# Performance work log

Hardware: AMD Instinct MI355X
Metric: run time of the kernel (lower is better)

Reference implementation:

```python
import jax, jax.numpy as jnp
import numpy as np

N_PP = 100000   # papers
N_A = 50000     # authors
N_AP = N_PP + N_A
DIM = 16
B = 8192        # sampled node set sizes
E = 500000      # edges per modality
ALPHA = 0.5
EPS = 1e-12


def _cdist(x, y):
    # Euclidean cdist via quadratic expansion (avoids [N,M,d] intermediate)
    sq = (jnp.sum(x * x, -1)[:, None] + jnp.sum(y * y, -1)[None, :]
          - 2.0 * x @ y.T)
    return jnp.sqrt(jnp.maximum(sq, EPS))


def _pdist(x, y):
    d = x - y
    return jnp.sqrt(jnp.sum(d * d, -1) + EPS)


def setup_inputs() -> dict:
    key = jax.random.key(0)
    ks = jax.random.split(key, 10)
    u = lambda k, s: jax.random.uniform(k, s, jnp.float32, -1.0, 1.0)  # 2*rand-1
    p = u(ks[0], (N_PP, DIM))
    p_star = u(ks[1], (N_PP, DIM))
    a = u(ks[2], (N_A, DIM))
    beta_ap = u(ks[3], (N_AP,))
    gamma_pp = u(ks[4], (2 * N_PP,))
    edges_pp = jax.random.randint(ks[5], (2, E), 0, N_PP, jnp.int32)
    e_ap0 = jax.random.randint(ks[6], (1, E), 0, N_PP, jnp.int32)
    e_ap1 = jax.random.randint(ks[7], (1, E), N_PP, N_AP, jnp.int32)
    edges_ap = jnp.concatenate([e_ap0, e_ap1], 0)
    p_star_nodes = jnp.sort(jax.random.randint(ks[8], (B,), 0, N_PP, jnp.int32))
    kk = jax.random.split(ks[9], 2)
    p_nodes = jax.random.randint(kk[0], (B,), 0, N_PP, jnp.int32)
    a_nodes = jax.random.randint(kk[1], (B,), N_PP, N_AP, jnp.int32)
    return {"p": p, "p_star": p_star, "a": a, "beta_ap": beta_ap,
            "gamma_pp": gamma_pp, "edges_pp": edges_pp, "edges_ap": edges_ap,
            "p_star_nodes": p_star_nodes, "p_nodes": p_nodes, "a_nodes": a_nodes}


def reference(p, p_star, a, beta_ap, gamma_pp,
              edges_pp, edges_ap, p_star_nodes, p_nodes, a_nodes):
    # ---- pp modality ----
    # link term over edges (edges[0]=p_star idx, edges[1]=p idx)
    link_pp = jnp.sum(gamma_pp[edges_pp[0]] + gamma_pp[edges_pp[1] + N_PP]
                      - _pdist(p_star[edges_pp[0]], p[edges_pp[1]]))
    # non-link term: [B_pstar, B_p] matrix, upper-triangular (k=1) masked sum
    g_ps = gamma_pp[p_star_nodes]                 # [B]
    g_p = gamma_pp[p_nodes + N_PP]                # [B]
    mat_pp = g_ps[:, None] + g_p[None, :]         # == gamma_mat.T in torch code
    dist_pp = _cdist(p_star[p_star_nodes], p[p_nodes])
    nonlink_pp = jnp.sum(jnp.triu(jnp.exp(mat_pp - dist_pp), k=1))
    nll_pp = -(link_pp - nonlink_pp)

    # ---- ap modality ----
    link_ap = jnp.sum(beta_ap[edges_ap[0]] + beta_ap[edges_ap[1]]
                      - _pdist(p_star[edges_ap[0]], a[edges_ap[1] - N_PP]))
    b_ps = beta_ap[p_star_nodes]
    b_a = beta_ap[a_nodes]
    mat_ap = b_ps[:, None] + b_a[None, :]         # == beta_mat.T
    dist_ap = _cdist(p_star[p_star_nodes], a[a_nodes - N_PP])
    nonlink_ap = jnp.sum(jnp.exp(mat_ap - dist_ap))
    nll_ap = -(link_ap - nonlink_ap)

    # average batch loss as in __train_one_batch
    loss = ALPHA * nll_pp / B + (1.0 - ALPHA) * nll_ap / B
    return loss
```

## Files before the change

### kernel.cpp

```cpp
#include <hip/hip_runtime.h>

#define N_PP 100000
#define N_A  50000
#define NEDGE 500000
#define BSZ 8192
#define TILE 128
#define SCALE 1.44269504088896f

#define GRID_F 1024
#define PAIR_JOBS 8192
#define EDGE_JOBS 489
#define NJOBS (PAIR_JOBS + EDGE_JOBS)

typedef __attribute__((ext_vector_type(8)))  short bf16x8;
typedef __attribute__((ext_vector_type(16))) float f32x16;
typedef __attribute__((ext_vector_type(4)))  float f32x4;
typedef unsigned short u16;

#if __has_builtin(__builtin_amdgcn_sqrtf)
#define FAST_SQRT(x) __builtin_amdgcn_sqrtf(x)
#else
#define FAST_SQRT(x) sqrtf(x)
#endif
#if __has_builtin(__builtin_amdgcn_exp2f)
#define FAST_EXP2(x) __builtin_amdgcn_exp2f(x)
#else
#define FAST_EXP2(x) exp2f(x)
#endif

__device__ __forceinline__ u16 f2bf(float f) {
    unsigned u = __builtin_bit_cast(unsigned, f);
    u += 0x7FFFu + ((u >> 16) & 1u);
    return (u16)(u >> 16);
}
__device__ __forceinline__ float bf2f(u16 s) {
    unsigned u = ((unsigned)s) << 16;
    return __builtin_bit_cast(float, u);
}

__device__ __forceinline__ bf16x8 load_frag_f32(const float* __restrict__ src) {
    float4 v0 = *(const float4*)src;
    float4 v1 = *(const float4*)(src + 4);
    bf16x8 f;
    f[0] = (short)f2bf(v0.x); f[1] = (short)f2bf(v0.y);
    f[2] = (short)f2bf(v0.z); f[3] = (short)f2bf(v0.w);
    f[4] = (short)f2bf(v1.x); f[5] = (short)f2bf(v1.y);
    f[6] = (short)f2bf(v1.z); f[7] = (short)f2bf(v1.w);
    return f;
}

__device__ __forceinline__ float pdist16_bf(const u16* __restrict__ xr,
                                            const u16* __restrict__ yr) {
    bf16x8 x0 = *(const bf16x8*)xr, x1 = *(const bf16x8*)(xr + 8);
    bf16x8 y0 = *(const bf16x8*)yr, y1 = *(const bf16x8*)(yr + 8);
    float d2 = 1e-12f;
#pragma unroll
    for (int i = 0; i < 8; ++i) {
        float dx = bf2f((u16)x0[i]) - bf2f((u16)y0[i]); d2 = fmaf(dx, dx, d2);
        float dy = bf2f((u16)x1[i]) - bf2f((u16)y1[i]); d2 = fmaf(dy, dy, d2);
    }
    return sqrtf(d2);
}

__device__ __forceinline__ float pdist16_f32(const float* __restrict__ xv,
                                             const float* __restrict__ yv) {
    float d2 = 1e-12f;
#pragma unroll
    for (int c = 0; c < 16; c += 4) {
        float4 xq = *(const float4*)(xv + c);
        float4 yq = *(const float4*)(yv + c);
        float dx = xq.x - yq.x; d2 = fmaf(dx, dx, d2);
        float dy = xq.y - yq.y; d2 = fmaf(dy, dy, d2);
        float dz = xq.z - yq.z; d2 = fmaf(dz, dz, d2);
        float dw = xq.w - yq.w; d2 = fmaf(dw, dw, d2);
    }
    return sqrtf(d2);
}

__global__ __launch_bounds__(256) void prep_kernel(
        const float* __restrict__ p, const float* __restrict__ p_star,
        const float* __restrict__ a, const float* __restrict__ beta,
        const float* __restrict__ gamma,
        const int* __restrict__ psn, const int* __restrict__ pn,
        const int* __restrict__ an,
        u16* __restrict__ ps_tab, u16* __restrict__ p_tab, u16* __restrict__ a_tab,
        u16* __restrict__ Xb, u16* __restrict__ Yp, u16* __restrict__ Ya,
        float* __restrict__ Xxx, float* __restrict__ Xg,
        float* __restrict__ Pyy, float* __restrict__ Pg,
        float* __restrict__ Ayy, float* __restrict__ Ag)
{
    const int NITEMS = 250000 + 3 * BSZ;
    for (int i = blockIdx.x * 256 + threadIdx.x; i < NITEMS; i += gridDim.x * 256) {
        if (i < 250000) {
            const float* src; u16* dst;
            if (i < 100000)      { src = p_star + (size_t)i * 16;       dst = ps_tab + (size_t)i * 16; }
            else if (i < 200000) { src = p + (size_t)(i - 100000) * 16; dst = p_tab + (size_t)(i - 100000) * 16; }
            else                 { src = a + (size_t)(i - 200000) * 16; dst = a_tab + (size_t)(i - 200000) * 16; }
            bf16x8 lo = load_frag_f32(src);
            bf16x8 hi = load_frag_f32(src + 8);
            *(bf16x8*)dst = lo;
            *(bf16x8*)(dst + 8) = hi;
        } else {
            const int j = i - 250000;
            const int which = j >> 13;
            const int r = j & (BSZ - 1);
            const float* src; float wsc; u16* drow; float* xxp; float* gp;
            if (which == 0) {
                int node = psn[r]; src = p_star + (size_t)node * 16;
                wsc = gamma[node] * SCALE; drow = Xb + (size_t)r * 16; xxp = Xxx; gp = Xg;
            } else if (which == 1) {
                int node = pn[r]; src = p + (size_t)node * 16;
                wsc = gamma[node + N_PP] * SCALE; drow = Yp + (size_t)r * 16; xxp = Pyy; gp = Pg;
            } else {
                int node = an[r]; src = a + (size_t)(node - N_PP) * 16;
                wsc = beta[node] * SCALE; drow = Ya + (size_t)r * 16; xxp = Ayy; gp = Ag;
            }
            bf16x8 lo = load_frag_f32(src);
            bf16x8 hi = load_frag_f32(src + 8);
            *(bf16x8*)drow = lo;
            *(bf16x8*)(drow + 8) = hi;
            float ss = 0.f;
#pragma unroll
            for (int c = 0; c < 8; ++c) {
                float q0 = bf2f((u16)lo[c]); ss = fmaf(q0, q0, ss);
                float q1 = bf2f((u16)hi[c]); ss = fmaf(q1, q1, ss);
            }
            xxp[r] = ss;
            gp[r] = wsc;
        }
    }
}

template <bool DIAG>
__device__ __forceinline__ float epi_rt(
        const f32x16& ca, const f32x16& cb,
        const float* __restrict__ xxg, const float* __restrict__ gxg,
        int rb, float yy0, float gy0, float yy1, float gy1,
        int cj0, int cj1)
{
    f32x4 xxq[4], gxq[4];
#pragma unroll
    for (int q = 0; q < 4; ++q) {
        xxq[q] = *(const f32x4*)&xxg[rb + q * 8];
        gxq[q] = *(const f32x4*)&gxg[rb + q * 8];
    }
    float s = 0.f;
#pragma unroll
    for (int q = 0; q < 4; ++q) {
#pragma unroll
        for (int j = 0; j < 4; ++j) {
            const int reg = q * 4 + j;
            float sxy = xxq[q][j];
            float gx  = gxq[q][j];
            float sq0 = fmaf(-2.f, ca[reg], sxy + yy0);
            float d0  = FAST_SQRT(fmaxf(sq0, 1e-12f));
            float v0  = FAST_EXP2(fmaf(-SCALE, d0, gx + gy0));
            float sq1 = fmaf(-2.f, cb[reg], sxy + yy1);
            float d1  = FAST_SQRT(fmaxf(sq1, 1e-12f));
            float v1  = FAST_EXP2(fmaf(-SCALE, d1, gx + gy1));
            if (DIAG) {
                int row = rb + q * 8 + j;
                v0 = (cj0 > row) ? v0 : 0.f;
                v1 = (cj1 > row) ? v1 : 0.f;
            }
            s += v0 + v1;
        }
    }
    return s;
}

template <bool PACKED>
__global__ __launch_bounds__(256) void fused_kernel(
        const float* __restrict__ p, const float* __restrict__ p_star,
        const float* __restrict__ a, const float* __restrict__ beta,
        const float* __restrict__ gamma,
        const int* __restrict__ edges_pp, const int* __restrict__ edges_ap,
        const int* __restrict__ psn, const int* __restrict__ pn,
        const int* __restrict__ an,
        const u16* __restrict__ ps_tab, const u16* __restrict__ p_tab,
        const u16* __restrict__ a_tab,
        const u16* __restrict__ Xb, const u16* __restrict__ Yp,
        const u16* __restrict__ Ya,
        const float* __restrict__ Xxx, const float* __restrict__ Xg,
        const float* __restrict__ Pyy, const float* __restrict__ Pg,
        const float* __restrict__ Ayy, const float* __restrict__ Ag,
        float* __restrict__ partials)
{
    const int t = threadIdx.x;
    const int l = t & 63, w = t >> 6;
    const int wr = w >> 1, wc = w & 1;
    const int l31 = l & 31, h = l >> 5;

    __shared__ float sxx[TILE], sgx[TILE], syy[TILE], sgy[TILE];
    __shared__ float red4[4][4];

    float s_ppl = 0.f, s_ppn = 0.f, s_apl = 0.f, s_apn = 0.f;

    for (int j = blockIdx.x; j < NJOBS; j += gridDim.x) {
        if (j < PAIR_JOBS) {
            const bool pp = (j < 4096);
            const int jj = pp ? j : j - 4096;
            const int bx = jj & 63, by = jj >> 6;
            if (pp && bx < by) continue;
            const bool diag = pp && (bx == by);

            bf16x8 aF0, aF1, bF0, bF1;
            const float* xxg; const float* gxg;
            float yy0, gy0, yy1, gy1;
            const int cj0 = wc * 64 + l31, cj1 = cj0 + 32;
            const int rb0 = wr * 64 + 4 * h, rb1 = rb0 + 32;

            if (PACKED) {
                const u16* Ytab = pp ? Yp : Ya;
                const float* yyP = (pp ? Pyy : Ayy) + bx * TILE;
                const float* gyP = (pp ? Pg  : Ag ) + bx * TILE;
                const int ar0 = by * TILE + wr * 64 + l31;
                const int bc0 = bx * TILE + wc * 64 + l31;
                aF0 = *(const bf16x8*)(Xb   + (size_t)ar0 * 16 + h * 8);
                aF1 = *(const bf16x8*)(Xb   + (size_t)(ar0 + 32) * 16 + h * 8);
                bF0 = *(const bf16x8*)(Ytab + (size_t)bc0 * 16 + h * 8);
                bF1 = *(const bf16x8*)(Ytab + (size_t)(bc0 + 32) * 16 + h * 8);
                xxg = Xxx + by * TILE;
                gxg = Xg  + by * TILE;
                yy0 = yyP[cj0]; gy0 = gyP[cj0];
                yy1 = yyP[cj1]; gy1 = gyP[cj1];
            } else {
                const float* Y  = pp ? p : a;
                const float* wv = pp ? gamma : beta;
                const int* yn   = pp ? pn : an;
                const int wyo   = pp ? N_PP : 0;
                const int yvo   = pp ? 0 : -N_PP;
                const int ar0 = by * TILE + wr * 64 + l31;
                const int an0 = psn[ar0], an1 = psn[ar0 + 32];
                aF0 = load_frag_f32(p_star + (size_t)an0 * 16 + h * 8);
                aF1 = load_frag_f32(p_star + (size_t)an1 * 16 + h * 8);
                const int bc0g = bx * TILE + wc * 64 + l31;
                const int bn0 = yn[bc0g], bn1 = yn[bc0g + 32];
                bF0 = load_frag_f32(Y + (size_t)(bn0 + yvo) * 16 + h * 8);
                bF1 = load_frag_f32(Y + (size_t)(bn1 + yvo) * 16 + h * 8);
                {
                    const bool isx = (t < 128);
                    const int  r   = isx ? t : t - 128;
                    const int  node = isx ? psn[by * TILE + r] : yn[bx * TILE + r];
                    const float* src = isx ? (p_star + (size_t)node * 16)
                                           : (Y + (size_t)(node + yvo) * 16);
                    float ss = 0.f;
#pragma unroll
                    for (int c = 0; c < 16; c += 4) {
                        float4 v = *(const float4*)(src + c);
                        float q0 = bf2f(f2bf(v.x)), q1 = bf2f(f2bf(v.y));
                        float q2 = bf2f(f2bf(v.z)), q3 = bf2f(f2bf(v.w));
                        ss = fmaf(q0, q0, ss); ss = fmaf(q1, q1, ss);
                        ss = fmaf(q2, q2, ss); ss = fmaf(q3, q3, ss);
                    }
                    if (isx) { sxx[r] = ss; sgx[r] = wv[node] * SCALE; }
                    else     { syy[r] = ss; sgy[r] = wv[node + wyo] * SCALE; }
                }
                __syncthreads();
                xxg = sxx; gxg = sgx;
                yy0 = syy[cj0]; gy0 = sgy[cj0];
                yy1 = syy[cj1]; gy1 = sgy[cj1];
            }

            f32x16 c00, c01, c10, c11;
#pragma unroll
            for (int i = 0; i < 16; ++i) { c00[i] = 0.f; c01[i] = 0.f; c10[i] = 0.f; c11[i] = 0.f; }
            c00 = __builtin_amdgcn_mfma_f32_32x32x16_bf16(aF0, bF0, c00, 0, 0, 0);
            c01 = __builtin_amdgcn_mfma_f32_32x32x16_bf16(aF0, bF1, c01, 0, 0, 0);
            c10 = __builtin_amdgcn_mfma_f32_32x32x16_bf16(aF1, bF0, c10, 0, 0, 0);
            c11 = __builtin_amdgcn_mfma_f32_32x32x16_bf16(aF1, bF1, c11, 0, 0, 0);

            float sum;
            if (diag) {
                sum = epi_rt<true >(c00, c01, xxg, gxg, rb0, yy0, gy0, yy1, gy1, cj0, cj1)
                    + epi_rt<true >(c10, c11, xxg, gxg, rb1, yy0, gy0, yy1, gy1, cj0, cj1);
            } else {
                sum = epi_rt<false>(c00, c01, xxg, gxg, rb0, yy0, gy0, yy1, gy1, cj0, cj1)
                    + epi_rt<false>(c10, c11, xxg, gxg, rb1, yy0, gy0, yy1, gy1, cj0, cj1);
            }
            if (pp) s_ppn += sum; else s_apn += sum;
            if (!PACKED) __syncthreads();
        } else {
            const int base = (j - PAIR_JOBS) * 1024;
#pragma unroll 2
            for (int k = 0; k < 4; ++k) {
                int i = base + k * 256 + t;
                if (i < NEDGE) {
                    int e0 = edges_pp[i], e1 = edges_pp[NEDGE + i];
                    int f0 = edges_ap[i], f1 = edges_ap[NEDGE + i];
                    if (PACKED) {
                        s_ppl += gamma[e0] + gamma[e1 + N_PP]
                               - pdist16_bf(ps_tab + (size_t)e0 * 16, p_tab + (size_t)e1 * 16);
                        s_apl += beta[f0] + beta[f1]
                               - pdist16_bf(ps_tab + (size_t)f0 * 16, a_tab + (size_t)(f1 - N_PP) * 16);
                    } else {
                        s_ppl += gamma[e0] + gamma[e1 + N_PP]
                               - pdist16_f32(p_star + (size_t)e0 * 16, p + (size_t)e1 * 16);
                        s_apl += beta[f0] + beta[f1]
                               - pdist16_f32(p_star + (size_t)f0 * 16, a + (size_t)(f1 - N_PP) * 16);
                    }
                }
            }
        }
    }

    float v4[4] = {s_ppl, s_ppn, s_apl, s_apn};
#pragma unroll
    for (int c = 0; c < 4; ++c) {
        float r = v4[c];
#pragma unroll
        for (int o = 32; o > 0; o >>= 1) r += __shfl_down(r, o, 64);
        if (l == 0) red4[w][c] = r;
    }
    __syncthreads();
    if (t < 4)
        partials[(size_t)blockIdx.x * 4 + t] =
            red4[0][t] + red4[1][t] + red4[2][t] + red4[3][t];
}

__global__ __launch_bounds__(256) void finalize_kernel(
        const float* __restrict__ partials, float* __restrict__ out)
{
    __shared__ double acc4[4];
    const int t = threadIdx.x;
    const int c = t >> 6, l = t & 63;
    double s = 0.0;
    for (int i = l; i < GRID_F; i += 64) s += (double)partials[(size_t)i * 4 + c];
#pragma unroll
    for (int o = 32; o > 0; o >>= 1) s += __shfl_down(s, o, 64);
    if (l == 0) acc4[c] = s;
    __syncthreads();
    if (t == 0) {
        double nll_pp = -(acc4[0] - acc4[1]);
        double nll_ap = -(acc4[2] - acc4[3]);
        out[0] = (float)(0.5 * nll_pp / (double)BSZ + 0.5 * nll_ap / (double)BSZ);
    }
}

extern "C" void kernel_launch(void* const* d_in, const int* in_sizes, int n_in,
                              void* d_out, int out_size, void* d_ws, size_t ws_size,
                              hipStream_t stream)
{
    const float* p       = (const float*)d_in[0];
    const float* p_star  = (const float*)d_in[1];
    const float* a       = (const float*)d_in[2];
    const float* beta    = (const float*)d_in[3];
    const float* gamma   = (const float*)d_in[4];
    const int* edges_pp  = (const int*)d_in[5];
    const int* edges_ap  = (const int*)d_in[6];
    const int* psn       = (const int*)d_in[7];
    const int* pn        = (const int*)d_in[8];
    const int* an        = (const int*)d_in[9];

    char* ws = (char*)d_ws;
    size_t off = 0;
    float* partials = (float*)(ws + off); off += (size_t)GRID_F * 4 * sizeof(float);
    u16* ps_tab = (u16*)(ws + off); off += (size_t)100000 * 32;
    u16* p_tab  = (u16*)(ws + off); off += (size_t)100000 * 32;
    u16* a_tab  = (u16*)(ws + off); off += (size_t)50000 * 32;
    u16* Xb     = (u16*)(ws + off); off += (size_t)BSZ * 32;
    u16* Yp     = (u16*)(ws + off); off += (size_t)BSZ * 32;
    u16* Ya     = (u16*)(ws + off); off += (size_t)BSZ * 32;
    float* Xxx  = (float*)(ws + off); off += BSZ * 4;
    float* Xg   = (float*)(ws + off); off += BSZ * 4;
    float* Pyy  = (float*)(ws + off); off += BSZ * 4;
    float* Pg   = (float*)(ws + off); off += BSZ * 4;
    float* Ayy  = (float*)(ws + off); off += BSZ * 4;
    float* Ag   = (float*)(ws + off); off += BSZ * 4;
    const bool packed = (ws_size >= off);

    if (packed) {
        prep_kernel<<<256, 256, 0, stream>>>(
            p, p_star, a, beta, gamma, psn, pn, an,
            ps_tab, p_tab, a_tab, Xb, Yp, Ya, Xxx, Xg, Pyy, Pg, Ayy, Ag);
        fused_kernel<true><<<GRID_F, 256, 0, stream>>>(
            p, p_star, a, beta, gamma, edges_pp, edges_ap, psn, pn, an,
            ps_tab, p_tab, a_tab, Xb, Yp, Ya, Xxx, Xg, Pyy, Pg, Ayy, Ag, partials);
    } else {
        fused_kernel<false><<<GRID_F, 256, 0, stream>>>(
            p, p_star, a, beta, gamma, edges_pp, edges_ap, psn, pn, an,
            nullptr, nullptr, nullptr, nullptr, nullptr, nullptr,
            nullptr, nullptr, nullptr, nullptr, nullptr, nullptr, partials);
    }

    finalize_kernel<<<1, 256, 0, stream>>>(partials, (float*)d_out);
}
```

Baseline: 85.83 us.

## Quantize gathered edge embeddings to int8 with sdot4 and rebalance job schedule

The edge-link term now gathers rows quantized to int8 (16 bytes per row instead of 32) and computes distances with sdot4 integer dot products, roughly halving gather traffic for the one million random edge lookups. The job list is reordered so edge jobs come first with smaller 512-edge chunks. The pp upper-triangle tiles are enumerated directly through a triangular index mapping instead of being skipped. Grid size doubles and launch bounds request 4 blocks per SM. Int8 quantization with scale 127 adds distance error of roughly 1e-2 per element, which may exceed the tolerance. Distances also lose the epsilon floor, so sqrt(0) is possible.

```diff
diff --git a/kernel.cpp b/kernel.cpp
--- a/kernel.cpp
+++ b/kernel.cpp
@@ -6,11 +6,14 @@
 #define BSZ 8192
 #define TILE 128
 #define SCALE 1.44269504088896f
-
-#define GRID_F 1024
-#define PAIR_JOBS 8192
-#define EDGE_JOBS 489
-#define NJOBS (PAIR_JOBS + EDGE_JOBS)
+#define QS 127.0f
+#define QSI (1.0f / 127.0f)
+
+#define GRID_F 2048
+#define EDGE_JOBS 977
+#define PP_JOBS 2080
+#define AP_JOBS 4096
+#define NJOBS (EDGE_JOBS + PP_JOBS + AP_JOBS)
 
 typedef __attribute__((ext_vector_type(8)))  short bf16x8;
 typedef __attribute__((ext_vector_type(16))) float f32x16;
@@ -49,17 +52,39 @@
     return f;
 }
 
-__device__ __forceinline__ float pdist16_bf(const u16* __restrict__ xr,
-                                            const u16* __restrict__ yr) {
-    bf16x8 x0 = *(const bf16x8*)xr, x1 = *(const bf16x8*)(xr + 8);
-    bf16x8 y0 = *(const bf16x8*)yr, y1 = *(const bf16x8*)(yr + 8);
-    float d2 = 1e-12f;
-#pragma unroll
-    for (int i = 0; i < 8; ++i) {
-        float dx = bf2f((u16)x0[i]) - bf2f((u16)y0[i]); d2 = fmaf(dx, dx, d2);
-        float dy = bf2f((u16)x1[i]) - bf2f((u16)y1[i]); d2 = fmaf(dy, dy, d2);
-    }
-    return sqrtf(d2);
+__device__ __forceinline__ int dot4i8(int a, int b, int c) {
+#if __has_builtin(__builtin_amdgcn_sdot4)
+    return __builtin_amdgcn_sdot4(a, b, c, false);
+#else
+    int s = c;
+#pragma unroll
+    for (int k = 0; k < 4; ++k) {
+        int av = (int)(signed char)(a >> (8 * k));
+        int bv = (int)(signed char)(b >> (8 * k));
+        s += av * bv;
+    }
+    return s;
+#endif
+}
+
+__device__ __forceinline__ float dist_i8(const int* __restrict__ ra,
+                                         const int* __restrict__ rb) {
+    int4 qa = *(const int4*)ra;
+    int4 qb = *(const int4*)rb;
+    int dot = dot4i8(qa.x, qb.x, 0);
+    dot = dot4i8(qa.y, qb.y, dot);
+    dot = dot4i8(qa.z, qb.z, dot);
+    dot = dot4i8(qa.w, qb.w, dot);
+    int na = dot4i8(qa.x, qa.x, 0);
+    na = dot4i8(qa.y, qa.y, na);
+    na = dot4i8(qa.z, qa.z, na);
+    na = dot4i8(qa.w, qa.w, na);
+    int nb = dot4i8(qb.x, qb.x, 0);
+    nb = dot4i8(qb.y, qb.y, nb);
+    nb = dot4i8(qb.z, qb.z, nb);
+    nb = dot4i8(qb.w, qb.w, nb);
+    int d2 = na + nb - 2 * dot;
+    return FAST_SQRT((float)d2) * QSI;
 }
 
 __device__ __forceinline__ float pdist16_f32(const float* __restrict__ xv,
@@ -77,13 +102,20 @@
     return sqrtf(d2);
 }
 
+__device__ __forceinline__ unsigned packq4(float a, float b, float c, float d) {
+    int qa = (int)rintf(a * QS), qb = (int)rintf(b * QS);
+    int qc = (int)rintf(c * QS), qd = (int)rintf(d * QS);
+    return (unsigned)(qa & 0xFF) | ((unsigned)(qb & 0xFF) << 8)
+         | ((unsigned)(qc & 0xFF) << 16) | ((unsigned)(qd & 0xFF) << 24);
+}
+
 __global__ __launch_bounds__(256) void prep_kernel(
         const float* __restrict__ p, const float* __restrict__ p_star,
         const float* __restrict__ a, const float* __restrict__ beta,
         const float* __restrict__ gamma,
         const int* __restrict__ psn, const int* __restrict__ pn,
         const int* __restrict__ an,
-        u16* __restrict__ ps_tab, u16* __restrict__ p_tab, u16* __restrict__ a_tab,
+        int* __restrict__ ps8, int* __restrict__ p8, int* __restrict__ a8,
         u16* __restrict__ Xb, u16* __restrict__ Yp, u16* __restrict__ Ya,
         float* __restrict__ Xxx, float* __restrict__ Xg,
         float* __restrict__ Pyy, float* __restrict__ Pg,
@@ -92,14 +124,20 @@
     const int NITEMS = 250000 + 3 * BSZ;
     for (int i = blockIdx.x * 256 + threadIdx.x; i < NITEMS; i += gridDim.x * 256) {
         if (i < 250000) {
-            const float* src; u16* dst;
-            if (i < 100000)      { src = p_star + (size_t)i * 16;       dst = ps_tab + (size_t)i * 16; }
-            else if (i < 200000) { src = p + (size_t)(i - 100000) * 16; dst = p_tab + (size_t)(i - 100000) * 16; }
-            else                 { src = a + (size_t)(i - 200000) * 16; dst = a_tab + (size_t)(i - 200000) * 16; }
-            bf16x8 lo = load_frag_f32(src);
-            bf16x8 hi = load_frag_f32(src + 8);
-            *(bf16x8*)dst = lo;
-            *(bf16x8*)(dst + 8) = hi;
+            const float* src; int* dst;
+            if (i < 100000)      { src = p_star + (size_t)i * 16;       dst = ps8 + (size_t)i * 4; }
+            else if (i < 200000) { src = p + (size_t)(i - 100000) * 16; dst = p8 + (size_t)(i - 100000) * 4; }
+            else                 { src = a + (size_t)(i - 200000) * 16; dst = a8 + (size_t)(i - 200000) * 4; }
+            float4 v0 = *(const float4*)src;
+            float4 v1 = *(const float4*)(src + 4);
+            float4 v2 = *(const float4*)(src + 8);
+            float4 v3 = *(const float4*)(src + 12);
+            int4 q;
+            q.x = (int)packq4(v0.x, v0.y, v0.z, v0.w);
+            q.y = (int)packq4(v1.x, v1.y, v1.z, v1.w);
+            q.z = (int)packq4(v2.x, v2.y, v2.z, v2.w);
+            q.w = (int)packq4(v3.x, v3.y, v3.z, v3.w);
+            *(int4*)dst = q;
         } else {
             const int j = i - 250000;
             const int which = j >> 13;
@@ -170,15 +208,15 @@
 }
 
 template <bool PACKED>
-__global__ __launch_bounds__(256) void fused_kernel(
+__global__ __launch_bounds__(256, 4) void fused_kernel(
         const float* __restrict__ p, const float* __restrict__ p_star,
         const float* __restrict__ a, const float* __restrict__ beta,
         const float* __restrict__ gamma,
         const int* __restrict__ edges_pp, const int* __restrict__ edges_ap,
         const int* __restrict__ psn, const int* __restrict__ pn,
         const int* __restrict__ an,
-        const u16* __restrict__ ps_tab, const u16* __restrict__ p_tab,
-        const u16* __restrict__ a_tab,
+        const int* __restrict__ ps8, const int* __restrict__ p8,
+        const int* __restrict__ a8,
         const u16* __restrict__ Xb, const u16* __restrict__ Yp,
         const u16* __restrict__ Ya,
         const float* __restrict__ Xxx, const float* __restrict__ Xg,
@@ -197,11 +235,43 @@
     float s_ppl = 0.f, s_ppn = 0.f, s_apl = 0.f, s_apn = 0.f;
 
     for (int j = blockIdx.x; j < NJOBS; j += gridDim.x) {
-        if (j < PAIR_JOBS) {
-            const bool pp = (j < 4096);
-            const int jj = pp ? j : j - 4096;
-            const int bx = jj & 63, by = jj >> 6;
-            if (pp && bx < by) continue;
+        if (j < EDGE_JOBS) {
+            const int base = j * 512;
+#pragma unroll
+            for (int k = 0; k < 2; ++k) {
+                int i = base + k * 256 + t;
+                if (i < NEDGE) {
+                    int e0 = __builtin_nontemporal_load(edges_pp + i);
+                    int e1 = __builtin_nontemporal_load(edges_pp + NEDGE + i);
+                    int f0 = __builtin_nontemporal_load(edges_ap + i);
+                    int f1 = __builtin_nontemporal_load(edges_ap + NEDGE + i);
+                    if (PACKED) {
+                        s_ppl += gamma[e0] + gamma[e1 + N_PP]
+                               - dist_i8(ps8 + (size_t)e0 * 4, p8 + (size_t)e1 * 4);
+                        s_apl += beta[f0] + beta[f1]
+                               - dist_i8(ps8 + (size_t)f0 * 4, a8 + (size_t)(f1 - N_PP) * 4);
+                    } else {
+                        s_ppl += gamma[e0] + gamma[e1 + N_PP]
+                               - pdist16_f32(p_star + (size_t)e0 * 16, p + (size_t)e1 * 16);
+                        s_apl += beta[f0] + beta[f1]
+                               - pdist16_f32(p_star + (size_t)f0 * 16, a + (size_t)(f1 - N_PP) * 16);
+                    }
+                }
+            }
+        } else {
+            const bool pp = (j < EDGE_JOBS + PP_JOBS);
+            int bx, by;
+            if (pp) {
+                int k = j - EDGE_JOBS;
+                float disc = sqrtf((float)(129 * 129 - 8 * k));
+                by = (int)((129.0f - disc) * 0.5f);
+                while (64 * by - (by * (by - 1)) / 2 > k) --by;
+                while (64 * (by + 1) - ((by + 1) * by) / 2 <= k) ++by;
+                bx = by + (k - (64 * by - (by * (by - 1)) / 2));
+            } else {
+                int k = j - EDGE_JOBS - PP_JOBS;
+                bx = k & 63; by = k >> 6;
+            }
             const bool diag = pp && (bx == by);
 
             bf16x8 aF0, aF1, bF0, bF1;
@@ -280,27 +350,6 @@
             }
             if (pp) s_ppn += sum; else s_apn += sum;
             if (!PACKED) __syncthreads();
-        } else {
-            const int base = (j - PAIR_JOBS) * 1024;
-#pragma unroll 2
-            for (int k = 0; k < 4; ++k) {
-                int i = base + k * 256 + t;
-                if (i < NEDGE) {
-                    int e0 = edges_pp[i], e1 = edges_pp[NEDGE + i];
-                    int f0 = edges_ap[i], f1 = edges_ap[NEDGE + i];
-                    if (PACKED) {
-                        s_ppl += gamma[e0] + gamma[e1 + N_PP]
-                               - pdist16_bf(ps_tab + (size_t)e0 * 16, p_tab + (size_t)e1 * 16);
-                        s_apl += beta[f0] + beta[f1]
-                               - pdist16_bf(ps_tab + (size_t)f0 * 16, a_tab + (size_t)(f1 - N_PP) * 16);
-                    } else {
-                        s_ppl += gamma[e0] + gamma[e1 + N_PP]
-                               - pdist16_f32(p_star + (size_t)e0 * 16, p + (size_t)e1 * 16);
-                        s_apl += beta[f0] + beta[f1]
-                               - pdist16_f32(p_star + (size_t)f0 * 16, a + (size_t)(f1 - N_PP) * 16);
-                    }
-                }
-            }
         }
     }
 
@@ -355,27 +404,27 @@
     char* ws = (char*)d_ws;
     size_t off = 0;
     float* partials = (float*)(ws + off); off += (size_t)GRID_F * 4 * sizeof(float);
-    u16* ps_tab = (u16*)(ws + off); off += (size_t)100000 * 32;
-    u16* p_tab  = (u16*)(ws + off); off += (size_t)100000 * 32;
-    u16* a_tab  = (u16*)(ws + off); off += (size_t)50000 * 32;
-    u16* Xb     = (u16*)(ws + off); off += (size_t)BSZ * 32;
-    u16* Yp     = (u16*)(ws + off); off += (size_t)BSZ * 32;
-    u16* Ya     = (u16*)(ws + off); off += (size_t)BSZ * 32;
-    float* Xxx  = (float*)(ws + off); off += BSZ * 4;
-    float* Xg   = (float*)(ws + off); off += BSZ * 4;
-    float* Pyy  = (float*)(ws + off); off += BSZ * 4;
-    float* Pg   = (float*)(ws + off); off += BSZ * 4;
-    float* Ayy  = (float*)(ws + off); off += BSZ * 4;
-    float* Ag   = (float*)(ws + off); off += BSZ * 4;
+    int* ps8 = (int*)(ws + off); off += (size_t)100000 * 16;
+    int* p8  = (int*)(ws + off); off += (size_t)100000 * 16;
+    int* a8  = (int*)(ws + off); off += (size_t)50000 * 16;
+    u16* Xb  = (u16*)(ws + off); off += (size_t)BSZ * 32;
+    u16* Yp  = (u16*)(ws + off); off += (size_t)BSZ * 32;
+    u16* Ya  = (u16*)(ws + off); off += (size_t)BSZ * 32;
+    float* Xxx = (float*)(ws + off); off += BSZ * 4;
+    float* Xg  = (float*)(ws + off); off += BSZ * 4;
+    float* Pyy = (float*)(ws + off); off += BSZ * 4;
+    float* Pg  = (float*)(ws + off); off += BSZ * 4;
+    float* Ayy = (float*)(ws + off); off += BSZ * 4;
+    float* Ag  = (float*)(ws + off); off += BSZ * 4;
     const bool packed = (ws_size >= off);
 
     if (packed) {
         prep_kernel<<<256, 256, 0, stream>>>(
             p, p_star, a, beta, gamma, psn, pn, an,
-            ps_tab, p_tab, a_tab, Xb, Yp, Ya, Xxx, Xg, Pyy, Pg, Ayy, Ag);
+            ps8, p8, a8, Xb, Yp, Ya, Xxx, Xg, Pyy, Pg, Ayy, Ag);
         fused_kernel<true><<<GRID_F, 256, 0, stream>>>(
             p, p_star, a, beta, gamma, edges_pp, edges_ap, psn, pn, an,
-            ps_tab, p_tab, a_tab, Xb, Yp, Ya, Xxx, Xg, Pyy, Pg, Ayy, Ag, partials);
+            ps8, p8, a8, Xb, Yp, Ya, Xxx, Xg, Pyy, Pg, Ayy, Ag, partials);
     } else {
         fused_kernel<false><<<GRID_F, 256, 0, stream>>>(
             p, p_star, a, beta, gamma, edges_pp, edges_ap, psn, pn, an,
```

Result: slower. 219.2 us (+155.4%).
